# Kernel optimization log

Hardware: AMD Instinct MI355X
Metric: run time of the kernel (lower is better)

The kernel has to match this reference:

```python
import jax, jax.numpy as jnp
import numpy as np

N = 50000
E = 800000
IN_F = 128
HID = 128
OUT_F = 64
MU = 2.0
EPS = 1e-12


def setup_inputs() -> dict:
    key = jax.random.key(0)
    ks = jax.random.split(key, 20)
    d = {}
    d["x"] = jax.random.normal(ks[0], (N, IN_F), dtype=jnp.float32)
    d["edge_src"] = jax.random.randint(ks[1], (E,), 0, N, dtype=jnp.int32)
    d["edge_dst"] = jax.random.randint(ks[2], (E,), 0, N, dtype=jnp.int32)
    d["edge_val"] = jax.random.uniform(ks[3], (E,), dtype=jnp.float32)
    # layer 0: in=128 -> pool=128 -> out=128 (activation=relu)
    s0 = 1.0 / np.sqrt(IN_F)
    d["pool_w0"] = jax.random.uniform(ks[4], (IN_F, IN_F), jnp.float32, -s0, s0)
    d["pool_b0"] = jax.random.uniform(ks[5], (IN_F,), jnp.float32, -s0, s0)
    d["fc1_w0"] = jax.random.uniform(ks[6], (HID, IN_F), jnp.float32, -s0, s0)
    d["fc1_b0"] = jax.random.uniform(ks[7], (HID,), jnp.float32, -s0, s0)
    d["fc2_w0"] = jax.random.uniform(ks[8], (HID, IN_F), jnp.float32, -s0, s0)
    d["fc2_b0"] = jax.random.uniform(ks[9], (HID,), jnp.float32, -s0, s0)
    # layer 1 (final): in=128 -> pool=128 -> out=64 (no activation)
    s1 = 1.0 / np.sqrt(HID)
    d["pool_w1"] = jax.random.uniform(ks[10], (HID, HID), jnp.float32, -s1, s1)
    d["pool_b1"] = jax.random.uniform(ks[11], (HID,), jnp.float32, -s1, s1)
    d["fc1_w1"] = jax.random.uniform(ks[12], (OUT_F, HID), jnp.float32, -s1, s1)
    d["fc1_b1"] = jax.random.uniform(ks[13], (OUT_F,), jnp.float32, -s1, s1)
    d["fc2_w1"] = jax.random.uniform(ks[14], (OUT_F, HID), jnp.float32, -s1, s1)
    d["fc2_b1"] = jax.random.uniform(ks[15], (OUT_F,), jnp.float32, -s1, s1)
    return d


def _sage_conv(x, src, dst, val, pw, pb, w1, b1, w2, b2, act):
    # L2-normalize rows (F.normalize(x, dim=1))
    xn = x / jnp.maximum(jnp.linalg.norm(x, axis=1, keepdims=True), EPS)
    h = jax.nn.relu(xn @ pw.T + pb)               # [N, pool]
    h_mu = h ** MU                                # elementwise pow
    # spmm(adj, h_mu): gather source rows, scale by edge weight, scatter-add to dst rows
    agg = jax.ops.segment_sum(h_mu[src] * val[:, None], dst, num_segments=N)
    agg = agg ** (1.0 / MU)                       # generalized-mean root
    out = (h @ w1.T + b1) + (agg @ w2.T + b2)
    return jax.nn.relu(out) if act else out


def reference(x, edge_src, edge_dst, edge_val,
              pool_w0, pool_b0, fc1_w0, fc1_b0, fc2_w0, fc2_b0,
              pool_w1, pool_b1, fc1_w1, fc1_b1, fc2_w1, fc2_b1):
    h = _sage_conv(x, edge_src, edge_dst, edge_val,
                   pool_w0, pool_b0, fc1_w0, fc1_b0, fc2_w0, fc2_b0, act=True)
    out = _sage_conv(h, edge_src, edge_dst, edge_val,
                     pool_w1, pool_b1, fc1_w1, fc1_b1, fc2_w1, fc2_b1, act=False)
    return out
```

## Files before the change

### kernel.cpp

```cpp
#include <hip/hip_runtime.h>

#define FF 128
#define BCAP 8192
#define CHUNK 4096
#define PITCH 136

typedef __attribute__((ext_vector_type(8))) short short8;
typedef __attribute__((ext_vector_type(4))) float f32x4;

__device__ __forceinline__ unsigned short bf16_rne(float f) {
    unsigned u = __float_as_uint(f);
    u += 0x7fffu + ((u >> 16) & 1u);
    return (unsigned short)(u >> 16);
}
__device__ __forceinline__ float bf16_to_f32(unsigned short h) {
    return __uint_as_float(((unsigned)h) << 16);
}

__global__ __launch_bounds__(256, 2)
void poolpartA_kernel(const float* __restrict__ x,
                      const unsigned short* __restrict__ Wh, const unsigned short* __restrict__ Wl,
                      const float* __restrict__ bias,
                      unsigned short* __restrict__ hout, unsigned short* __restrict__ hsqout,
                      const int* __restrict__ esrc, const int* __restrict__ edst,
                      const float* __restrict__ eval,
                      int* __restrict__ bucket_cnt, int2* __restrict__ ebuf,
                      int N, int E, int nchunks)
{
    __shared__ alignas(16) char smem[37888];
    const int t = threadIdx.x;

    if (blockIdx.x < nchunks) {
        int* cnt   = (int*)smem;
        int* sc    = cnt + 256;
        int* excl  = sc + 256;
        int* cur   = excl + 256;
        int* gbase = cur + 256;
        int2* staged = (int2*)(smem + 5 * 256 * 4);
        const int e0 = blockIdx.x * CHUNK;
        const int n  = min(CHUNK, E - e0);

        cnt[t] = 0;
        __syncthreads();
        for (int i = t; i < n; i += 256)
            atomicAdd(&cnt[((unsigned)edst[e0 + i]) >> 8], 1);
        __syncthreads();

        sc[t] = cnt[t];
        __syncthreads();
        #pragma unroll
        for (int off = 1; off < 256; off <<= 1) {
            int v = (t >= off) ? sc[t - off] : 0;
            __syncthreads();
            sc[t] += v;
            __syncthreads();
        }
        excl[t] = sc[t] - cnt[t];
        cur[t]  = excl[t];
        if (cnt[t] > 0) gbase[t] = atomicAdd(&bucket_cnt[t], cnt[t]);
        __syncthreads();

        for (int i = t; i < n; i += 256) {
            int d = edst[e0 + i];
            int s = esrc[e0 + i];
            float v = eval[e0 + i];
            int b = ((unsigned)d) >> 8;
            int slot = atomicAdd(&cur[b], 1);
            staged[slot] = make_int2((s & 0xffff) | (d << 16), __float_as_int(v));
        }
        __syncthreads();

        for (int p = t; p < n; p += 256) {
            int2 ent = staged[p];
            int b = ((unsigned)ent.x) >> 24;
            int gpos = gbase[b] + (p - excl[b]);
            ebuf[(size_t)b * BCAP + gpos] = ent;
        }
    } else {
        unsigned short* sX = (unsigned short*)smem;
        float* sNorm = (float*)(smem + 64 * PITCH * 2);
        const int tile = blockIdx.x - nchunks;

        #pragma unroll
        for (int rg = 0; rg < 2; ++rg) {
            const int row = rg * 32 + (t >> 3);
            const int c0  = (t & 7) * 16;
            const int n   = tile * 64 + row;
            const int base = row * PITCH + c0;
            float v[16];
            if (n < N) {
                const float4* p = (const float4*)(x + (size_t)n * FF + c0);
                #pragma unroll
                for (int i = 0; i < 4; ++i) {
                    float4 q = p[i];
                    v[4*i] = q.x; v[4*i+1] = q.y; v[4*i+2] = q.z; v[4*i+3] = q.w;
                }
            } else {
                #pragma unroll
                for (int i = 0; i < 16; ++i) v[i] = 0.f;
            }
            float ss = 0.f;
            #pragma unroll
            for (int i = 0; i < 16; ++i) ss = fmaf(v[i], v[i], ss);
            union { unsigned short u[8]; short8 s; } h0, h1;
            #pragma unroll
            for (int i = 0; i < 8; ++i) {
                h0.u[i] = bf16_rne(v[i]);
                h1.u[i] = bf16_rne(v[8 + i]);
            }
            *(short8*)&sX[base]     = h0.s;
            *(short8*)&sX[base + 8] = h1.s;
            ss += __shfl_xor(ss, 1);
            ss += __shfl_xor(ss, 2);
            ss += __shfl_xor(ss, 4);
            if ((t & 7) == 0) sNorm[row] = 1.0f / fmaxf(sqrtf(ss), 1e-12f);
        }
        __syncthreads();

        const int lane = t & 63, wave = t >> 6;
        const int quad = lane >> 4, l16 = lane & 15;

        short8 Bh[2][4], Bl[2][4];
        #pragma unroll
        for (int c = 0; c < 2; ++c) {
            const int jt = 2 * wave + c;
            #pragma unroll
            for (int tt = 0; tt < 4; ++tt) {
                const size_t o = ((size_t)(jt * 4 + tt) * 64 + lane) * 8;
                Bh[c][tt] = *(const short8*)&Wh[o];
                Bl[c][tt] = *(const short8*)&Wl[o];
            }
        }

        f32x4 acc[4][2];
        #pragma unroll
        for (int r = 0; r < 4; ++r)
            #pragma unroll
            for (int c = 0; c < 2; ++c) {
                f32x4 z = {0.f, 0.f, 0.f, 0.f};
                acc[r][c] = z;
            }

        #pragma unroll
        for (int tt = 0; tt < 4; ++tt) {
            short8 Ah[4];
            #pragma unroll
            for (int r = 0; r < 4; ++r)
                Ah[r] = *(const short8*)&sX[(r * 16 + l16) * PITCH + tt * 32 + quad * 8];
            #pragma unroll
            for (int c = 0; c < 2; ++c)
                #pragma unroll
                for (int r = 0; r < 4; ++r) {
                    acc[r][c] = __builtin_amdgcn_mfma_f32_16x16x32_bf16(Ah[r], Bh[c][tt], acc[r][c], 0, 0, 0);
                    acc[r][c] = __builtin_amdgcn_mfma_f32_16x16x32_bf16(Ah[r], Bl[c][tt], acc[r][c], 0, 0, 0);
                }
        }

        #pragma unroll
        for (int c = 0; c < 2; ++c) {
            const int j = (2 * wave + c) * 16 + l16;
            const float bj = bias[j];
            #pragma unroll
            for (int r = 0; r < 4; ++r) {
                #pragma unroll
                for (int g = 0; g < 4; ++g) {
                    const int nl = r * 16 + quad * 4 + g;
                    const int n = tile * 64 + nl;
                    if (n < N) {
                        float s = sNorm[nl];
                        float val = fmaf(acc[r][c][g], s, bj);
                        val = fmaxf(val, 0.f);
                        hout  [(size_t)n * FF + j] = bf16_rne(val);
                        hsqout[(size_t)n * FF + j] = bf16_rne(val * val);
                    }
                }
            }
        }
    }
}

__global__ __launch_bounds__(256, 2)
void pool_mfma_bf16(const unsigned short* __restrict__ xin,
                    const unsigned short* __restrict__ Wh, const unsigned short* __restrict__ Wl,
                    const float* __restrict__ bias,
                    unsigned short* __restrict__ hout, unsigned short* __restrict__ hsqout, int N)
{
    __shared__ unsigned short sX[64 * PITCH];
    __shared__ float sNorm[64];

    const int tid  = threadIdx.x;
    const int tile = blockIdx.x;

    #pragma unroll
    for (int rg = 0; rg < 2; ++rg) {
        const int row = rg * 32 + (tid >> 3);
        const int c0  = (tid & 7) * 16;
        const int n   = tile * 64 + row;
        const int base = row * PITCH + c0;
        union { short8 s; unsigned short u[8]; } a, b;
        short8 z = {0,0,0,0,0,0,0,0};
        a.s = z; b.s = z;
        if (n < N) {
            const short8* p = (const short8*)(xin + (size_t)n * FF + c0);
            a.s = p[0]; b.s = p[1];
        }
        float ss = 0.f;
        #pragma unroll
        for (int i = 0; i < 8; ++i) {
            float fa = bf16_to_f32(a.u[i]);
            float fb = bf16_to_f32(b.u[i]);
            ss = fmaf(fa, fa, fmaf(fb, fb, ss));
        }
        *(short8*)&sX[base]     = a.s;
        *(short8*)&sX[base + 8] = b.s;
        ss += __shfl_xor(ss, 1);
        ss += __shfl_xor(ss, 2);
        ss += __shfl_xor(ss, 4);
        if ((tid & 7) == 0) sNorm[row] = 1.0f / fmaxf(sqrtf(ss), 1e-12f);
    }
    __syncthreads();

    const int lane = tid & 63, wave = tid >> 6;
    const int quad = lane >> 4, l16 = lane & 15;

    short8 Bh[2][4], Bl[2][4];
    #pragma unroll
    for (int c = 0; c < 2; ++c) {
        const int jt = 2 * wave + c;
        #pragma unroll
        for (int t = 0; t < 4; ++t) {
            const size_t o = ((size_t)(jt * 4 + t) * 64 + lane) * 8;
            Bh[c][t] = *(const short8*)&Wh[o];
            Bl[c][t] = *(const short8*)&Wl[o];
        }
    }

    f32x4 acc[4][2];
    #pragma unroll
    for (int r = 0; r < 4; ++r)
        #pragma unroll
        for (int c = 0; c < 2; ++c) {
            f32x4 z = {0.f, 0.f, 0.f, 0.f};
            acc[r][c] = z;
        }

    #pragma unroll
    for (int t = 0; t < 4; ++t) {
        short8 Ah[4];
        #pragma unroll
        for (int r = 0; r < 4; ++r)
            Ah[r] = *(const short8*)&sX[(r * 16 + l16) * PITCH + t * 32 + quad * 8];
        #pragma unroll
        for (int c = 0; c < 2; ++c)
            #pragma unroll
            for (int r = 0; r < 4; ++r) {
                acc[r][c] = __builtin_amdgcn_mfma_f32_16x16x32_bf16(Ah[r], Bh[c][t], acc[r][c], 0, 0, 0);
                acc[r][c] = __builtin_amdgcn_mfma_f32_16x16x32_bf16(Ah[r], Bl[c][t], acc[r][c], 0, 0, 0);
            }
    }

    #pragma unroll
    for (int c = 0; c < 2; ++c) {
        const int j = (2 * wave + c) * 16 + l16;
        const float bj = bias[j];
        #pragma unroll
        for (int r = 0; r < 4; ++r) {
            #pragma unroll
            for (int g = 0; g < 4; ++g) {
                const int nl = r * 16 + quad * 4 + g;
                const int n = tile * 64 + nl;
                if (n < N) {
                    float s = sNorm[nl];
                    float val = fmaf(acc[r][c][g], s, bj);
                    val = fmaxf(val, 0.f);
                    hout  [(size_t)n * FF + j] = bf16_rne(val);
                    hsqout[(size_t)n * FF + j] = bf16_rne(val * val);
                }
            }
        }
    }
}

template<int OUT, int RELU, int OUTBF16>
__global__ __launch_bounds__(256, 2)
void mm2_mfma(const unsigned short* __restrict__ hin,
              const unsigned short* __restrict__ aggh,
              const unsigned short* __restrict__ W1h, const unsigned short* __restrict__ W1l,
              const unsigned short* __restrict__ W2h, const unsigned short* __restrict__ W2l,
              const float* __restrict__ b1, const float* __restrict__ b2,
              void* __restrict__ out_, int N)
{
    __shared__ unsigned short sH [64 * PITCH];
    __shared__ unsigned short sAh[64 * PITCH];

    const int tid  = threadIdx.x;
    const int tile = blockIdx.x;

    #pragma unroll
    for (int rg = 0; rg < 2; ++rg) {
        const int row = rg * 32 + (tid >> 3);
        const int c0  = (tid & 7) * 16;
        const int n   = tile * 64 + row;
        const int base = row * PITCH + c0;
        short8 z = {0,0,0,0,0,0,0,0};
        short8 a = z, b = z, c = z, d = z;
        if (n < N) {
            const short8* ph = (const short8*)(hin  + (size_t)n * FF + c0);
            const short8* pa = (const short8*)(aggh + (size_t)n * FF + c0);
            a = ph[0]; b = ph[1];
            c = pa[0]; d = pa[1];
        }
        *(short8*)&sH [base]     = a;
        *(short8*)&sH [base + 8] = b;
        *(short8*)&sAh[base]     = c;
        *(short8*)&sAh[base + 8] = d;
    }
    __syncthreads();

    const int lane = tid & 63, wave = tid >> 6;
    const int quad = lane >> 4, l16 = lane & 15;
    constexpr int CT = (OUT == 128) ? 2 : 1;

    short8 B1hf[CT][4], B1lf[CT][4], B2hf[CT][4], B2lf[CT][4];
    #pragma unroll
    for (int c = 0; c < CT; ++c) {
        const int jt = (OUT == 128) ? (2 * wave + c) : wave;
        #pragma unroll
        for (int t = 0; t < 4; ++t) {
            const size_t o = ((size_t)(jt * 4 + t) * 64 + lane) * 8;
            B1hf[c][t] = *(const short8*)&W1h[o];
            B1lf[c][t] = *(const short8*)&W1l[o];
            B2hf[c][t] = *(const short8*)&W2h[o];
            B2lf[c][t] = *(const short8*)&W2l[o];
        }
    }

    f32x4 acc[4][CT];
    #pragma unroll
    for (int r = 0; r < 4; ++r)
        #pragma unroll
        for (int c = 0; c < CT; ++c) {
            f32x4 z = {0.f, 0.f, 0.f, 0.f};
            acc[r][c] = z;
        }

    #pragma unroll
    for (int t = 0; t < 4; ++t) {
        short8 Hf[4], AH[4];
        #pragma unroll
        for (int r = 0; r < 4; ++r) {
            const int off = (r * 16 + l16) * PITCH + t * 32 + quad * 8;
            Hf[r] = *(const short8*)&sH[off];
            AH[r] = *(const short8*)&sAh[off];
        }
        #pragma unroll
        for (int c = 0; c < CT; ++c)
            #pragma unroll
            for (int r = 0; r < 4; ++r) {
                acc[r][c] = __builtin_amdgcn_mfma_f32_16x16x32_bf16(Hf[r], B1hf[c][t], acc[r][c], 0, 0, 0);
                acc[r][c] = __builtin_amdgcn_mfma_f32_16x16x32_bf16(Hf[r], B1lf[c][t], acc[r][c], 0, 0, 0);
                acc[r][c] = __builtin_amdgcn_mfma_f32_16x16x32_bf16(AH[r], B2hf[c][t], acc[r][c], 0, 0, 0);
                acc[r][c] = __builtin_amdgcn_mfma_f32_16x16x32_bf16(AH[r], B2lf[c][t], acc[r][c], 0, 0, 0);
            }
    }

    #pragma unroll
    for (int c = 0; c < CT; ++c) {
        const int jt = (OUT == 128) ? (2 * wave + c) : wave;
        const int j = jt * 16 + l16;
        const float bj = b1[j] + b2[j];
        #pragma unroll
        for (int r = 0; r < 4; ++r) {
            #pragma unroll
            for (int g = 0; g < 4; ++g) {
                const int n = tile * 64 + r * 16 + quad * 4 + g;
                if (n < N) {
                    float val = acc[r][c][g] + bj;
                    if constexpr (RELU) val = fmaxf(val, 0.f);
                    if constexpr (OUTBF16)
                        ((unsigned short*)out_)[(size_t)n * OUT + j] = bf16_rne(val);
                    else
                        ((float*)out_)[(size_t)n * OUT + j] = val;
                }
            }
        }
    }
}

struct WPack {
    const float* src[6];
    unsigned short* hi[6];
    unsigned short* lo[6];
    int n[6];
};

__global__ __launch_bounds__(256)
void wprep_kernel(WPack p, int* __restrict__ bucket_cnt)
{
    if (blockIdx.x == 0) bucket_cnt[threadIdx.x] = 0;
    int id = blockIdx.x * 256 + threadIdx.x;
    #pragma unroll
    for (int i = 0; i < 6; ++i) {
        if (id < p.n[i]) {
            float f = p.src[i][id];
            unsigned short h = bf16_rne(f);
            const int j = id >> 7, k = id & 127;
            const int jt = j >> 4, l16 = j & 15;
            const int t = k >> 5, quad = (k >> 3) & 3, j8 = k & 7;
            const size_t o = ((size_t)((jt * 4 + t) * 4 + quad) * 16 + l16) * 8 + j8;
            p.hi[i][o] = h;
            p.lo[i][o] = bf16_rne(f - bf16_to_f32(h));
            return;
        }
        id -= p.n[i];
    }
}

__global__ __launch_bounds__(256)
void partB_kernel(const int* __restrict__ bucket_cnt, const int2* __restrict__ ebuf,
                  int* __restrict__ offsets, int2* __restrict__ edata,
                  int N, int E, int nbuck)
{
    __shared__ int pre[256], hist[256], sc[256], excl[256], cur[256];
    const int t = threadIdx.x;
    const int b = blockIdx.x;

    pre[t] = (t < nbuck) ? bucket_cnt[t] : 0;
    __syncthreads();
    #pragma unroll
    for (int off = 1; off < 256; off <<= 1) {
        int v = (t >= off) ? pre[t - off] : 0;
        __syncthreads();
        pre[t] += v;
        __syncthreads();
    }
    const int base = (b == 0) ? 0 : pre[b - 1];
    const int cnt  = pre[b] - base;

    hist[t] = 0;
    __syncthreads();
    const int2* ib = ebuf + (size_t)b * BCAP;
    for (int i = t; i < cnt; i += 256)
        atomicAdd(&hist[(((unsigned)ib[i].x) >> 16) & 255], 1);
    __syncthreads();

    sc[t] = hist[t];
    __syncthreads();
    #pragma unroll
    for (int off = 1; off < 256; off <<= 1) {
        int v = (t >= off) ? sc[t - off] : 0;
        __syncthreads();
        sc[t] += v;
        __syncthreads();
    }
    excl[t] = sc[t] - hist[t];
    cur[t]  = excl[t];

    const int node = b * 256 + t;
    if (node <= N) offsets[node] = base + excl[t];
    __syncthreads();

    for (int i = t; i < cnt; i += 256) {
        int2 ent = ib[i];
        int l = (((unsigned)ent.x) >> 16) & 255;
        int pos = base + atomicAdd(&cur[l], 1);
        edata[pos] = make_int2(ent.x & 0xffff, ent.y);
    }
}

__device__ __forceinline__ void fma4(float4& a, float v, uint2 u) {
    a.x = fmaf(v, __uint_as_float(u.x << 16), a.x);
    a.y = fmaf(v, __uint_as_float(u.x & 0xffff0000u), a.y);
    a.z = fmaf(v, __uint_as_float(u.y << 16), a.z);
    a.w = fmaf(v, __uint_as_float(u.y & 0xffff0000u), a.w);
}

__global__ __launch_bounds__(256)
void agg_kernel(const unsigned short* __restrict__ hsq, const int* __restrict__ offsets,
                const int2* __restrict__ edata,
                unsigned short* __restrict__ aggh, int N)
{
    const int w = blockIdx.x * 8 + (threadIdx.x >> 5);
    if (w >= N) return;
    const int l = threadIdx.x & 31;
    const size_t fo = (size_t)(l * 4);
    int e = offsets[w];
    const int end = offsets[w + 1];

    float4 a0 = {0,0,0,0}, a1 = {0,0,0,0}, a2 = {0,0,0,0}, a3 = {0,0,0,0};

    if ((e & 1) && e < end) {
        int2 ed = edata[e];
        uint2 u = *(const uint2*)&hsq[(size_t)ed.x * FF + fo];
        fma4(a0, __int_as_float(ed.y), u);
        ++e;
    }
    for (; e + 3 < end; e += 4) {
        int4 p0 = *(const int4*)&edata[e];
        int4 p1 = *(const int4*)&edata[e + 2];
        uint2 u0 = *(const uint2*)&hsq[(size_t)p0.x * FF + fo];
        uint2 u1 = *(const uint2*)&hsq[(size_t)p0.z * FF + fo];
        uint2 u2 = *(const uint2*)&hsq[(size_t)p1.x * FF + fo];
        uint2 u3 = *(const uint2*)&hsq[(size_t)p1.z * FF + fo];
        fma4(a0, __int_as_float(p0.y), u0);
        fma4(a1, __int_as_float(p0.w), u1);
        fma4(a2, __int_as_float(p1.y), u2);
        fma4(a3, __int_as_float(p1.w), u3);
    }
    if (e + 1 < end) {
        int4 p = *(const int4*)&edata[e];
        uint2 u0 = *(const uint2*)&hsq[(size_t)p.x * FF + fo];
        uint2 u1 = *(const uint2*)&hsq[(size_t)p.z * FF + fo];
        fma4(a0, __int_as_float(p.y), u0);
        fma4(a1, __int_as_float(p.w), u1);
        e += 2;
    }
    if (e < end) {
        int2 ed = edata[e];
        uint2 u = *(const uint2*)&hsq[(size_t)ed.x * FF + fo];
        fma4(a0, __int_as_float(ed.y), u);
    }

    float4 r;
    r.x = sqrtf(a0.x + a1.x + a2.x + a3.x);
    r.y = sqrtf(a0.y + a1.y + a2.y + a3.y);
    r.z = sqrtf(a0.z + a1.z + a2.z + a3.z);
    r.w = sqrtf(a0.w + a1.w + a2.w + a3.w);

    uint2 hv = { (unsigned)bf16_rne(r.x) | ((unsigned)bf16_rne(r.y) << 16),
                 (unsigned)bf16_rne(r.z) | ((unsigned)bf16_rne(r.w) << 16) };
    *(uint2*)&aggh[(size_t)w * FF + fo] = hv;
}

extern "C" void kernel_launch(void* const* d_in, const int* in_sizes, int n_in,
                              void* d_out, int out_size, void* d_ws, size_t ws_size,
                              hipStream_t stream) {
    const float* x    = (const float*)d_in[0];
    const int*   esrc = (const int*)d_in[1];
    const int*   edst = (const int*)d_in[2];
    const float* eval = (const float*)d_in[3];
    const float* pw0  = (const float*)d_in[4];
    const float* pb0  = (const float*)d_in[5];
    const float* f1w0 = (const float*)d_in[6];
    const float* f1b0 = (const float*)d_in[7];
    const float* f2w0 = (const float*)d_in[8];
    const float* f2b0 = (const float*)d_in[9];
    const float* pw1  = (const float*)d_in[10];
    const float* pb1  = (const float*)d_in[11];
    const float* f1w1 = (const float*)d_in[12];
    const float* f1b1 = (const float*)d_in[13];
    const float* f2w1 = (const float*)d_in[14];
    const float* f2b1 = (const float*)d_in[15];
    float* out = (float*)d_out;

    const int N = in_sizes[0] / FF;
    const int E = in_sizes[1];
    const int nbuck = (N + 255) / 256;

    char* ws = (char*)d_ws;
    const size_t planesz = (size_t)N * FF * 2;
    const size_t A = 256;
    size_t off = 0;
    unsigned short* h    = (unsigned short*)(ws + off); off += (planesz + A - 1) / A * A;
    unsigned short* hsq  = (unsigned short*)(ws + off); off += (planesz + A - 1) / A * A;
    unsigned short* aggh = (unsigned short*)(ws + off); off += (planesz + A - 1) / A * A;
    unsigned short* x1   = (unsigned short*)(ws + off); off += (planesz + A - 1) / A * A;
    int* offsets = (int*)(ws + off); off += ((size_t)(N + 1) * 4 + A - 1) / A * A;
    int* bucket_cnt = (int*)(ws + off); off += (size_t)256 * 4;
    int2* ebuf  = (int2*)(ws + off); off += (size_t)nbuck * BCAP * 8;
    int2* edata = (int2*)(ws + off); off += (size_t)E * 8;
    const int wsz[6] = {128 * FF, 128 * FF, 128 * FF, 128 * FF, 64 * FF, 64 * FF};
    unsigned short* whi[6];
    unsigned short* wlo[6];
    for (int i = 0; i < 6; ++i) {
        whi[i] = (unsigned short*)(ws + off); off += (size_t)wsz[i] * 2;
        wlo[i] = (unsigned short*)(ws + off); off += (size_t)wsz[i] * 2;
    }

    WPack pack;
    const float* wsrc[6] = {pw0, f1w0, f2w0, pw1, f1w1, f2w1};
    int wtotal = 0;
    for (int i = 0; i < 6; ++i) {
        pack.src[i] = wsrc[i]; pack.hi[i] = whi[i]; pack.lo[i] = wlo[i]; pack.n[i] = wsz[i];
        wtotal += wsz[i];
    }

    const int ntiles     = (N + 63) / 64;
    const int nodeblocks = (N + 7) / 8;
    const int nchunks    = (E + CHUNK - 1) / CHUNK;
    dim3 B(256);

    wprep_kernel<<<(wtotal + 255) / 256, B, 0, stream>>>(pack, bucket_cnt);

    poolpartA_kernel<<<nchunks + ntiles, B, 0, stream>>>(
        x, whi[0], wlo[0], pb0, h, hsq, esrc, edst, eval, bucket_cnt, ebuf, N, E, nchunks);

    partB_kernel<<<nbuck, B, 0, stream>>>(bucket_cnt, ebuf, offsets, edata, N, E, nbuck);

    agg_kernel<<<nodeblocks, B, 0, stream>>>(hsq, offsets, edata, aggh, N);

    mm2_mfma<128, 1, 1><<<ntiles, B, 0, stream>>>(h, aggh, whi[1], wlo[1], whi[2], wlo[2], f1b0, f2b0, x1, N);

    pool_mfma_bf16<<<ntiles, B, 0, stream>>>(x1, whi[3], wlo[3], pb1, h, hsq, N);

    agg_kernel<<<nodeblocks, B, 0, stream>>>(hsq, offsets, edata, aggh, N);

    mm2_mfma<64, 0, 0><<<ntiles, B, 0, stream>>>(h, aggh, whi[4], wlo[4], whi[5], wlo[5], f1b1, f2b1, out, N);
}
```

Measured before the change: 236.8 us.

## Fuse gather-aggregation, fc matmuls and next pool into one per-layer kernel

Merges the edge aggregation, the fc1/fc2 matmuls and the next layer's pooling matmul into a single fused_layer kernel per layer, so aggh and x1 never round-trip through global memory and three launches are removed. The h/hsq outputs are staged through shared memory so global stores are coalesced 16-byte writes rather than scattered 2-byte ones. In exchange, each 64-row tile now does its aggregation with one 32-lane group per node over 8 sub-iterations. That cuts gather parallelism and occupancy compared with the old standalone agg kernel, and the fused kernel uses more shared memory.

Measured after the change: 285.8 us. 1.21x slower.

```diff
diff --git a/kernel.cpp b/kernel.cpp
--- a/kernel.cpp
+++ b/kernel.cpp
@@ -79,6 +79,7 @@
     } else {
         unsigned short* sX = (unsigned short*)smem;
         float* sNorm = (float*)(smem + 64 * PITCH * 2);
+        unsigned short* sOutQ = (unsigned short*)(smem + 64 * PITCH * 2 + 256);
         const int tile = blockIdx.x - nchunks;
 
         #pragma unroll
@@ -156,6 +157,7 @@
                 }
         }
 
+        __syncthreads();
         #pragma unroll
         for (int c = 0; c < 2; ++c) {
             const int j = (2 * wave + c) * 16 + l16;
@@ -165,155 +167,135 @@
                 #pragma unroll
                 for (int g = 0; g < 4; ++g) {
                     const int nl = r * 16 + quad * 4 + g;
-                    const int n = tile * 64 + nl;
-                    if (n < N) {
-                        float s = sNorm[nl];
-                        float val = fmaf(acc[r][c][g], s, bj);
-                        val = fmaxf(val, 0.f);
-                        hout  [(size_t)n * FF + j] = bf16_rne(val);
-                        hsqout[(size_t)n * FF + j] = bf16_rne(val * val);
-                    }
-                }
-            }
-        }
-    }
-}
-
+                    float s = sNorm[nl];
+                    float val = fmaf(acc[r][c][g], s, bj);
+                    val = fmaxf(val, 0.f);
+                    sX   [nl * PITCH + j] = bf16_rne(val);
+                    sOutQ[nl * PITCH + j] = bf16_rne(val * val);
+                }
+            }
+        }
+        __syncthreads();
+        #pragma unroll
+        for (int rg = 0; rg < 2; ++rg) {
+            const int row = rg * 32 + (t >> 3);
+            const int c0  = (t & 7) * 16;
+            const int n   = tile * 64 + row;
+            if (n < N) {
+                const int base = row * PITCH + c0;
+                *(short8*)&hout  [(size_t)n * FF + c0]     = *(short8*)&sX[base];
+                *(short8*)&hout  [(size_t)n * FF + c0 + 8] = *(short8*)&sX[base + 8];
+                *(short8*)&hsqout[(size_t)n * FF + c0]     = *(short8*)&sOutQ[base];
+                *(short8*)&hsqout[(size_t)n * FF + c0 + 8] = *(short8*)&sOutQ[base + 8];
+            }
+        }
+    }
+}
+
+__device__ __forceinline__ void fma4(float4& a, float v, uint2 u) {
+    a.x = fmaf(v, __uint_as_float(u.x << 16), a.x);
+    a.y = fmaf(v, __uint_as_float(u.x & 0xffff0000u), a.y);
+    a.z = fmaf(v, __uint_as_float(u.y << 16), a.z);
+    a.w = fmaf(v, __uint_as_float(u.y & 0xffff0000u), a.w);
+}
+
+template<int OUT, int POOLFUSE>
 __global__ __launch_bounds__(256, 2)
-void pool_mfma_bf16(const unsigned short* __restrict__ xin,
-                    const unsigned short* __restrict__ Wh, const unsigned short* __restrict__ Wl,
-                    const float* __restrict__ bias,
-                    unsigned short* __restrict__ hout, unsigned short* __restrict__ hsqout, int N)
+void fused_layer(const unsigned short* __restrict__ hin,
+                 const unsigned short* __restrict__ hsqin,
+                 const int* __restrict__ offsets, const int2* __restrict__ edata,
+                 const unsigned short* __restrict__ W1h, const unsigned short* __restrict__ W1l,
+                 const unsigned short* __restrict__ W2h, const unsigned short* __restrict__ W2l,
+                 const float* __restrict__ b1, const float* __restrict__ b2,
+                 const unsigned short* __restrict__ PWh, const unsigned short* __restrict__ PWl,
+                 const float* __restrict__ pb,
+                 float* __restrict__ out,
+                 unsigned short* __restrict__ hout, unsigned short* __restrict__ hsqout,
+                 int N)
 {
-    __shared__ unsigned short sX[64 * PITCH];
+    __shared__ unsigned short sH[64 * PITCH];
+    __shared__ unsigned short sA[64 * PITCH];
+    __shared__ unsigned short sX1[POOLFUSE ? (64 * PITCH) : 1];
     __shared__ float sNorm[64];
 
     const int tid  = threadIdx.x;
     const int tile = blockIdx.x;
 
+    short8 hreg[2][2];
     #pragma unroll
     for (int rg = 0; rg < 2; ++rg) {
         const int row = rg * 32 + (tid >> 3);
         const int c0  = (tid & 7) * 16;
         const int n   = tile * 64 + row;
-        const int base = row * PITCH + c0;
-        union { short8 s; unsigned short u[8]; } a, b;
         short8 z = {0,0,0,0,0,0,0,0};
-        a.s = z; b.s = z;
+        hreg[rg][0] = z; hreg[rg][1] = z;
         if (n < N) {
-            const short8* p = (const short8*)(xin + (size_t)n * FF + c0);
-            a.s = p[0]; b.s = p[1];
-        }
-        float ss = 0.f;
-        #pragma unroll
-        for (int i = 0; i < 8; ++i) {
-            float fa = bf16_to_f32(a.u[i]);
-            float fb = bf16_to_f32(b.u[i]);
-            ss = fmaf(fa, fa, fmaf(fb, fb, ss));
-        }
-        *(short8*)&sX[base]     = a.s;
-        *(short8*)&sX[base + 8] = b.s;
-        ss += __shfl_xor(ss, 1);
-        ss += __shfl_xor(ss, 2);
-        ss += __shfl_xor(ss, 4);
-        if ((tid & 7) == 0) sNorm[row] = 1.0f / fmaxf(sqrtf(ss), 1e-12f);
-    }
-    __syncthreads();
-
-    const int lane = tid & 63, wave = tid >> 6;
-    const int quad = lane >> 4, l16 = lane & 15;
-
-    short8 Bh[2][4], Bl[2][4];
-    #pragma unroll
-    for (int c = 0; c < 2; ++c) {
-        const int jt = 2 * wave + c;
-        #pragma unroll
-        for (int t = 0; t < 4; ++t) {
-            const size_t o = ((size_t)(jt * 4 + t) * 64 + lane) * 8;
-            Bh[c][t] = *(const short8*)&Wh[o];
-            Bl[c][t] = *(const short8*)&Wl[o];
-        }
-    }
-
-    f32x4 acc[4][2];
-    #pragma unroll
-    for (int r = 0; r < 4; ++r)
-        #pragma unroll
-        for (int c = 0; c < 2; ++c) {
-            f32x4 z = {0.f, 0.f, 0.f, 0.f};
-            acc[r][c] = z;
-        }
-
-    #pragma unroll
-    for (int t = 0; t < 4; ++t) {
-        short8 Ah[4];
-        #pragma unroll
-        for (int r = 0; r < 4; ++r)
-            Ah[r] = *(const short8*)&sX[(r * 16 + l16) * PITCH + t * 32 + quad * 8];
-        #pragma unroll
-        for (int c = 0; c < 2; ++c)
-            #pragma unroll
-            for (int r = 0; r < 4; ++r) {
-                acc[r][c] = __builtin_amdgcn_mfma_f32_16x16x32_bf16(Ah[r], Bh[c][t], acc[r][c], 0, 0, 0);
-                acc[r][c] = __builtin_amdgcn_mfma_f32_16x16x32_bf16(Ah[r], Bl[c][t], acc[r][c], 0, 0, 0);
-            }
-    }
-
-    #pragma unroll
-    for (int c = 0; c < 2; ++c) {
-        const int j = (2 * wave + c) * 16 + l16;
-        const float bj = bias[j];
-        #pragma unroll
-        for (int r = 0; r < 4; ++r) {
-            #pragma unroll
-            for (int g = 0; g < 4; ++g) {
-                const int nl = r * 16 + quad * 4 + g;
-                const int n = tile * 64 + nl;
-                if (n < N) {
-                    float s = sNorm[nl];
-                    float val = fmaf(acc[r][c][g], s, bj);
-                    val = fmaxf(val, 0.f);
-                    hout  [(size_t)n * FF + j] = bf16_rne(val);
-                    hsqout[(size_t)n * FF + j] = bf16_rne(val * val);
-                }
-            }
-        }
-    }
-}
-
-template<int OUT, int RELU, int OUTBF16>
-__global__ __launch_bounds__(256, 2)
-void mm2_mfma(const unsigned short* __restrict__ hin,
-              const unsigned short* __restrict__ aggh,
-              const unsigned short* __restrict__ W1h, const unsigned short* __restrict__ W1l,
-              const unsigned short* __restrict__ W2h, const unsigned short* __restrict__ W2l,
-              const float* __restrict__ b1, const float* __restrict__ b2,
-              void* __restrict__ out_, int N)
-{
-    __shared__ unsigned short sH [64 * PITCH];
-    __shared__ unsigned short sAh[64 * PITCH];
-
-    const int tid  = threadIdx.x;
-    const int tile = blockIdx.x;
+            const short8* p = (const short8*)(hin + (size_t)n * FF + c0);
+            hreg[rg][0] = p[0]; hreg[rg][1] = p[1];
+        }
+    }
+
+    {
+        const int g = tid >> 5, l = tid & 31;
+        const size_t fo = (size_t)(l * 4);
+        #pragma unroll 1
+        for (int sub = 0; sub < 8; ++sub) {
+            const int nl = sub * 8 + g;
+            const int w = tile * 64 + nl;
+            uint2 hv = {0u, 0u};
+            if (w < N) {
+                int e = offsets[w];
+                const int end = offsets[w + 1];
+                float4 a0 = {0,0,0,0}, a1 = {0,0,0,0}, a2 = {0,0,0,0}, a3 = {0,0,0,0};
+                if ((e & 1) && e < end) {
+                    int2 ed = edata[e];
+                    uint2 u = *(const uint2*)&hsqin[(size_t)ed.x * FF + fo];
+                    fma4(a0, __int_as_float(ed.y), u);
+                    ++e;
+                }
+                for (; e + 3 < end; e += 4) {
+                    int4 p0 = *(const int4*)&edata[e];
+                    int4 p1 = *(const int4*)&edata[e + 2];
+                    uint2 u0 = *(const uint2*)&hsqin[(size_t)p0.x * FF + fo];
+                    uint2 u1 = *(const uint2*)&hsqin[(size_t)p0.z * FF + fo];
+                    uint2 u2 = *(const uint2*)&hsqin[(size_t)p1.x * FF + fo];
+                    uint2 u3 = *(const uint2*)&hsqin[(size_t)p1.z * FF + fo];
+                    fma4(a0, __int_as_float(p0.y), u0);
+                    fma4(a1, __int_as_float(p0.w), u1);
+                    fma4(a2, __int_as_float(p1.y), u2);
+                    fma4(a3, __int_as_float(p1.w), u3);
+                }
+                if (e + 1 < end) {
+                    int4 p = *(const int4*)&edata[e];
+                    uint2 u0 = *(const uint2*)&hsqin[(size_t)p.x * FF + fo];
+                    uint2 u1 = *(const uint2*)&hsqin[(size_t)p.z * FF + fo];
+                    fma4(a0, __int_as_float(p.y), u0);
+                    fma4(a1, __int_as_float(p.w), u1);
+                    e += 2;
+                }
+                if (e < end) {
+                    int2 ed = edata[e];
+                    uint2 u = *(const uint2*)&hsqin[(size_t)ed.x * FF + fo];
+                    fma4(a0, __int_as_float(ed.y), u);
+                }
+                float4 r;
+                r.x = sqrtf(a0.x + a1.x + a2.x + a3.x);
+                r.y = sqrtf(a0.y + a1.y + a2.y + a3.y);
+                r.z = sqrtf(a0.z + a1.z + a2.z + a3.z);
+                r.w = sqrtf(a0.w + a1.w + a2.w + a3.w);
+                hv.x = (unsigned)bf16_rne(r.x) | ((unsigned)bf16_rne(r.y) << 16);
+                hv.y = (unsigned)bf16_rne(r.z) | ((unsigned)bf16_rne(r.w) << 16);
+            }
+            *(uint2*)&sA[nl * PITCH + l * 4] = hv;
+        }
+    }
 
     #pragma unroll
     for (int rg = 0; rg < 2; ++rg) {
         const int row = rg * 32 + (tid >> 3);
-        const int c0  = (tid & 7) * 16;
-        const int n   = tile * 64 + row;
-        const int base = row * PITCH + c0;
-        short8 z = {0,0,0,0,0,0,0,0};
-        short8 a = z, b = z, c = z, d = z;
-        if (n < N) {
-            const short8* ph = (const short8*)(hin  + (size_t)n * FF + c0);
-            const short8* pa = (const short8*)(aggh + (size_t)n * FF + c0);
-            a = ph[0]; b = ph[1];
-            c = pa[0]; d = pa[1];
-        }
-        *(short8*)&sH [base]     = a;
-        *(short8*)&sH [base + 8] = b;
-        *(short8*)&sAh[base]     = c;
-        *(short8*)&sAh[base + 8] = d;
+        const int base = row * PITCH + (tid & 7) * 16;
+        *(short8*)&sH[base]     = hreg[rg][0];
+        *(short8*)&sH[base + 8] = hreg[rg][1];
     }
     __syncthreads();
 
@@ -351,7 +333,7 @@
         for (int r = 0; r < 4; ++r) {
             const int off = (r * 16 + l16) * PITCH + t * 32 + quad * 8;
             Hf[r] = *(const short8*)&sH[off];
-            AH[r] = *(const short8*)&sAh[off];
+            AH[r] = *(const short8*)&sA[off];
         }
         #pragma unroll
         for (int c = 0; c < CT; ++c)
@@ -364,24 +346,125 @@
             }
     }
 
-    #pragma unroll
-    for (int c = 0; c < CT; ++c) {
-        const int jt = (OUT == 128) ? (2 * wave + c) : wave;
-        const int j = jt * 16 + l16;
-        const float bj = b1[j] + b2[j];
-        #pragma unroll
-        for (int r = 0; r < 4; ++r) {
-            #pragma unroll
-            for (int g = 0; g < 4; ++g) {
-                const int n = tile * 64 + r * 16 + quad * 4 + g;
-                if (n < N) {
-                    float val = acc[r][c][g] + bj;
-                    if constexpr (RELU) val = fmaxf(val, 0.f);
-                    if constexpr (OUTBF16)
-                        ((unsigned short*)out_)[(size_t)n * OUT + j] = bf16_rne(val);
-                    else
-                        ((float*)out_)[(size_t)n * OUT + j] = val;
-                }
+    if constexpr (!POOLFUSE) {
+        #pragma unroll
+        for (int c = 0; c < CT; ++c) {
+            const int jt = (OUT == 128) ? (2 * wave + c) : wave;
+            const int j = jt * 16 + l16;
+            const float bj = b1[j] + b2[j];
+            #pragma unroll
+            for (int r = 0; r < 4; ++r) {
+                #pragma unroll
+                for (int g = 0; g < 4; ++g) {
+                    const int n = tile * 64 + r * 16 + quad * 4 + g;
+                    if (n < N)
+                        out[(size_t)n * OUT + j] = acc[r][c][g] + bj;
+                }
+            }
+        }
+    } else {
+        #pragma unroll
+        for (int c = 0; c < CT; ++c) {
+            const int j = (2 * wave + c) * 16 + l16;
+            const float bj = b1[j] + b2[j];
+            #pragma unroll
+            for (int r = 0; r < 4; ++r) {
+                #pragma unroll
+                for (int g = 0; g < 4; ++g) {
+                    const int nl = r * 16 + quad * 4 + g;
+                    float val = fmaxf(acc[r][c][g] + bj, 0.f);
+                    sX1[nl * PITCH + j] = bf16_rne(val);
+                }
+            }
+        }
+        __syncthreads();
+
+        #pragma unroll
+        for (int rg = 0; rg < 2; ++rg) {
+            const int row = rg * 32 + (tid >> 3);
+            const int c0  = (tid & 7) * 16;
+            union { short8 s; unsigned short u[8]; } a, b;
+            a.s = *(short8*)&sX1[row * PITCH + c0];
+            b.s = *(short8*)&sX1[row * PITCH + c0 + 8];
+            float ss = 0.f;
+            #pragma unroll
+            for (int i = 0; i < 8; ++i) {
+                float fa = bf16_to_f32(a.u[i]);
+                float fb = bf16_to_f32(b.u[i]);
+                ss = fmaf(fa, fa, fmaf(fb, fb, ss));
+            }
+            ss += __shfl_xor(ss, 1);
+            ss += __shfl_xor(ss, 2);
+            ss += __shfl_xor(ss, 4);
+            if ((tid & 7) == 0) sNorm[row] = 1.0f / fmaxf(sqrtf(ss), 1e-12f);
+        }
+        __syncthreads();
+
+        short8 Ph[2][4], Pl[2][4];
+        #pragma unroll
+        for (int c = 0; c < 2; ++c) {
+            const int jt = 2 * wave + c;
+            #pragma unroll
+            for (int t = 0; t < 4; ++t) {
+                const size_t o = ((size_t)(jt * 4 + t) * 64 + lane) * 8;
+                Ph[c][t] = *(const short8*)&PWh[o];
+                Pl[c][t] = *(const short8*)&PWl[o];
+            }
+        }
+
+        f32x4 acc2[4][2];
+        #pragma unroll
+        for (int r = 0; r < 4; ++r)
+            #pragma unroll
+            for (int c = 0; c < 2; ++c) {
+                f32x4 z = {0.f, 0.f, 0.f, 0.f};
+                acc2[r][c] = z;
+            }
+
+        #pragma unroll
+        for (int t = 0; t < 4; ++t) {
+            short8 Ah[4];
+            #pragma unroll
+            for (int r = 0; r < 4; ++r)
+                Ah[r] = *(const short8*)&sX1[(r * 16 + l16) * PITCH + t * 32 + quad * 8];
+            #pragma unroll
+            for (int c = 0; c < 2; ++c)
+                #pragma unroll
+                for (int r = 0; r < 4; ++r) {
+                    acc2[r][c] = __builtin_amdgcn_mfma_f32_16x16x32_bf16(Ah[r], Ph[c][t], acc2[r][c], 0, 0, 0);
+                    acc2[r][c] = __builtin_amdgcn_mfma_f32_16x16x32_bf16(Ah[r], Pl[c][t], acc2[r][c], 0, 0, 0);
+                }
+        }
+
+        __syncthreads();
+        #pragma unroll
+        for (int c = 0; c < 2; ++c) {
+            const int j = (2 * wave + c) * 16 + l16;
+            const float pbj = pb[j];
+            #pragma unroll
+            for (int r = 0; r < 4; ++r) {
+                #pragma unroll
+                for (int g = 0; g < 4; ++g) {
+                    const int nl = r * 16 + quad * 4 + g;
+                    float s = sNorm[nl];
+                    float val = fmaxf(fmaf(acc2[r][c][g], s, pbj), 0.f);
+                    sH[nl * PITCH + j] = bf16_rne(val);
+                    sA[nl * PITCH + j] = bf16_rne(val * val);
+                }
+            }
+        }
+        __syncthreads();
+        #pragma unroll
+        for (int rg = 0; rg < 2; ++rg) {
+            const int row = rg * 32 + (tid >> 3);
+            const int c0  = (tid & 7) * 16;
+            const int n   = tile * 64 + row;
+            if (n < N) {
+                const int base = row * PITCH + c0;
+                *(short8*)&hout  [(size_t)n * FF + c0]     = *(short8*)&sH[base];
+                *(short8*)&hout  [(size_t)n * FF + c0 + 8] = *(short8*)&sH[base + 8];
+                *(short8*)&hsqout[(size_t)n * FF + c0]     = *(short8*)&sA[base];
+                *(short8*)&hsqout[(size_t)n * FF + c0 + 8] = *(short8*)&sA[base + 8];
             }
         }
     }
@@ -466,70 +549,6 @@
         int pos = base + atomicAdd(&cur[l], 1);
         edata[pos] = make_int2(ent.x & 0xffff, ent.y);
     }
-}
-
-__device__ __forceinline__ void fma4(float4& a, float v, uint2 u) {
-    a.x = fmaf(v, __uint_as_float(u.x << 16), a.x);
-    a.y = fmaf(v, __uint_as_float(u.x & 0xffff0000u), a.y);
-    a.z = fmaf(v, __uint_as_float(u.y << 16), a.z);
-    a.w = fmaf(v, __uint_as_float(u.y & 0xffff0000u), a.w);
-}
-
-__global__ __launch_bounds__(256)
-void agg_kernel(const unsigned short* __restrict__ hsq, const int* __restrict__ offsets,
-                const int2* __restrict__ edata,
-                unsigned short* __restrict__ aggh, int N)
-{
-    const int w = blockIdx.x * 8 + (threadIdx.x >> 5);
-    if (w >= N) return;
-    const int l = threadIdx.x & 31;
-    const size_t fo = (size_t)(l * 4);
-    int e = offsets[w];
-    const int end = offsets[w + 1];
-
-    float4 a0 = {0,0,0,0}, a1 = {0,0,0,0}, a2 = {0,0,0,0}, a3 = {0,0,0,0};
-
-    if ((e & 1) && e < end) {
-        int2 ed = edata[e];
-        uint2 u = *(const uint2*)&hsq[(size_t)ed.x * FF + fo];
-        fma4(a0, __int_as_float(ed.y), u);
-        ++e;
-    }
-    for (; e + 3 < end; e += 4) {
-        int4 p0 = *(const int4*)&edata[e];
-        int4 p1 = *(const int4*)&edata[e + 2];
-        uint2 u0 = *(const uint2*)&hsq[(size_t)p0.x * FF + fo];
-        uint2 u1 = *(const uint2*)&hsq[(size_t)p0.z * FF + fo];
-        uint2 u2 = *(const uint2*)&hsq[(size_t)p1.x * FF + fo];
-        uint2 u3 = *(const uint2*)&hsq[(size_t)p1.z * FF + fo];
-        fma4(a0, __int_as_float(p0.y), u0);
-        fma4(a1, __int_as_float(p0.w), u1);
-        fma4(a2, __int_as_float(p1.y), u2);
-        fma4(a3, __int_as_float(p1.w), u3);
-    }
-    if (e + 1 < end) {
-        int4 p = *(const int4*)&edata[e];
-        uint2 u0 = *(const uint2*)&hsq[(size_t)p.x * FF + fo];
-        uint2 u1 = *(const uint2*)&hsq[(size_t)p.z * FF + fo];
-        fma4(a0, __int_as_float(p.y), u0);
-        fma4(a1, __int_as_float(p.w), u1);
-        e += 2;
-    }
-    if (e < end) {
-        int2 ed = edata[e];
-        uint2 u = *(const uint2*)&hsq[(size_t)ed.x * FF + fo];
-        fma4(a0, __int_as_float(ed.y), u);
-    }
-
-    float4 r;
-    r.x = sqrtf(a0.x + a1.x + a2.x + a3.x);
-    r.y = sqrtf(a0.y + a1.y + a2.y + a3.y);
-    r.z = sqrtf(a0.z + a1.z + a2.z + a3.z);
-    r.w = sqrtf(a0.w + a1.w + a2.w + a3.w);
-
-    uint2 hv = { (unsigned)bf16_rne(r.x) | ((unsigned)bf16_rne(r.y) << 16),
-                 (unsigned)bf16_rne(r.z) | ((unsigned)bf16_rne(r.w) << 16) };
-    *(uint2*)&aggh[(size_t)w * FF + fo] = hv;
 }
 
 extern "C" void kernel_launch(void* const* d_in, const int* in_sizes, int n_in,
@@ -563,8 +582,8 @@
     size_t off = 0;
     unsigned short* h    = (unsigned short*)(ws + off); off += (planesz + A - 1) / A * A;
     unsigned short* hsq  = (unsigned short*)(ws + off); off += (planesz + A - 1) / A * A;
-    unsigned short* aggh = (unsigned short*)(ws + off); off += (planesz + A - 1) / A * A;
-    unsigned short* x1   = (unsigned short*)(ws + off); off += (planesz + A - 1) / A * A;
+    unsigned short* h2   = (unsigned short*)(ws + off); off += (planesz + A - 1) / A * A;
+    unsigned short* hsq2 = (unsigned short*)(ws + off); off += (planesz + A - 1) / A * A;
     int* offsets = (int*)(ws + off); off += ((size_t)(N + 1) * 4 + A - 1) / A * A;
     int* bucket_cnt = (int*)(ws + off); off += (size_t)256 * 4;
     int2* ebuf  = (int2*)(ws + off); off += (size_t)nbuck * BCAP * 8;
@@ -585,9 +604,8 @@
         wtotal += wsz[i];
     }
 
-    const int ntiles     = (N + 63) / 64;
-    const int nodeblocks = (N + 7) / 8;
-    const int nchunks    = (E + CHUNK - 1) / CHUNK;
+    const int ntiles  = (N + 63) / 64;
+    const int nchunks = (E + CHUNK - 1) / CHUNK;
     dim3 B(256);
 
     wprep_kernel<<<(wtotal + 255) / 256, B, 0, stream>>>(pack, bucket_cnt);
@@ -597,13 +615,15 @@
 
     partB_kernel<<<nbuck, B, 0, stream>>>(bucket_cnt, ebuf, offsets, edata, N, E, nbuck);
 
-    agg_kernel<<<nodeblocks, B, 0, stream>>>(hsq, offsets, edata, aggh, N);
-
-    mm2_mfma<128, 1, 1><<<ntiles, B, 0, stream>>>(h, aggh, whi[1], wlo[1], whi[2], wlo[2], f1b0, f2b0, x1, N);
-
-    pool_mfma_bf16<<<ntiles, B, 0, stream>>>(x1, whi[3], wlo[3], pb1, h, hsq, N);
-
-    agg_kernel<<<nodeblocks, B, 0, stream>>>(hsq, offsets, edata, aggh, N);
-
-    mm2_mfma<64, 0, 0><<<ntiles, B, 0, stream>>>(h, aggh, whi[4], wlo[4], whi[5], wlo[5], f1b1, f2b1, out, N);
-}
+    fused_layer<128, 1><<<ntiles, B, 0, stream>>>(
+        h, hsq, offsets, edata,
+        whi[1], wlo[1], whi[2], wlo[2], f1b0, f2b0,
+        whi[3], wlo[3], pb1,
+        (float*)nullptr, h2, hsq2, N);
+
+    fused_layer<64, 0><<<ntiles, B, 0, stream>>>(
+        h2, hsq2, offsets, edata,
+        whi[4], wlo[4], whi[5], wlo[5], f1b1, f2b1,
+        (const unsigned short*)nullptr, (const unsigned short*)nullptr, (const float*)nullptr,
+        out, (unsigned short*)nullptr, (unsigned short*)nullptr, N);
+}
```
